# Performance work log

Hardware: AMD Instinct MI355X
Metric: run time of the kernel (lower is better)

The kernel has to match this reference:

```python
import jax, jax.numpy as jnp
import numpy as np

PI = 3.14159  # module uses this truncated pi
CX, CY, FOCAL = 256.0, 256.0, 608.365


def _sh_basis(depth):
    # depth: [B, H, W] (already rescaled to (d+1)/2)
    B, H, W = depth.shape
    gx = jnp.arange(W, dtype=depth.dtype)
    gy = jnp.arange(H, dtype=depth.dtype)
    xx, yy = jnp.meshgrid(gx, gy)            # 'xy' indexing, matches np.meshgrid
    xx = (xx - CX) / FOCAL * depth           # [B,H,W]
    yy = (yy - CY) / FOCAL * depth
    p = jnp.stack([xx, yy, depth], axis=-1)  # [B,H,W,3]

    p_ctr = p[:, 1:-1, 1:-1]
    vw = p_ctr - p[:, 1:-1, 2:]
    vs = p[:, 2:, 1:-1] - p_ctr
    ve = p_ctr - p[:, 1:-1, :-2]
    vn = p[:, :-2, 1:-1] - p_ctr
    normal = jnp.cross(vw, vs) + jnp.cross(ve, vn)     # [B,H-2,W-2,3]
    nmag = jnp.sqrt(jnp.sum(normal * normal, axis=-1)) # [B,H-2,W-2]
    nunit = normal / nmag[..., None]

    pad3 = ((0, 0), (1, 1), (1, 1), (0, 0))
    pad2 = ((0, 0), (1, 1), (1, 1))
    n_raw = jnp.pad(normal, pad3)   # UNNORMALIZED normals (faithful to source: normal_*_pad)
    n_u = jnp.pad(nunit, pad3)      # normalized normals (n_x/n_y/n_z)
    mag = jnp.pad(nmag, pad2)

    nx, ny, nz = n_u[..., 0], n_u[..., 1], n_u[..., 2]
    x2, y2, z2 = nx * nx, ny * ny, nz * nz
    xy, xz, yz = nx * ny, nx * nz, ny * nz

    c0 = PI * np.sqrt(1.0 / (4 * PI))
    c1 = 2 * PI / 3.0 * np.sqrt(3.0 / (4 * PI))
    c2 = PI / 4.0 * 0.5 * np.sqrt(5.0 / (4 * PI))
    c3 = PI / 4.0 * 3.0 * np.sqrt(5.0 / (12 * PI))
    c4 = PI / 4.0 * 3.0 * np.sqrt(5.0 / (48 * PI))

    N = jnp.stack([
        c0 * mag,
        c1 * n_raw[..., 2],
        c1 * n_raw[..., 0],
        c1 * n_raw[..., 1],
        c2 * (2 * z2 - x2 - y2) * mag,
        c3 * xz * mag,
        c3 * yz * mag,
        c4 * (x2 - y2) * mag,
        c3 * xy * mag,
    ], axis=-1)  # [B,H,W,9]
    return N


def setup_inputs() -> dict:
    key = jax.random.key(0)
    k1, k2, k3 = jax.random.split(key, 3)
    B, H, W = 8, 512, 512
    input_img = jax.random.normal(k1, (B, 3, H, W), dtype=jnp.float32)
    depth_target = jax.random.uniform(k2, (B, 1, H, W), dtype=jnp.float32)
    albedo = jax.random.uniform(k3, (B, 3, H, W), dtype=jnp.float32)
    return {"input_img": input_img, "depth_target": depth_target, "albedo": albedo}


def reference(input_img, depth_target, albedo):
    B, C, H, W = input_img.shape
    P = H * W
    depth = (depth_target + 1.0) / 2.0           # [B,1,H,W]
    img = (input_img + 1.0) / 2.0                # [B,3,H,W]
    # mask: binary, 1 wherever channel-0 of scaled image is nonzero
    mask = (img[:, :1] != 0).astype(img.dtype)   # [B,1,H,W]
    img = img * mask

    N = _sh_basis(depth[:, 0])                   # [B,H,W,9]
    A_fla = N.reshape(B, P, 9)

    rhoc_mask = (albedo * mask).reshape(B, 3, P)
    # Faithful bug reproduction: the source loop overwrites rhoc_N each channel
    # iteration, so only the LAST channel (index 2) of rhoc_mask is used for all
    # three least-squares systems.
    A = A_fla * rhoc_mask[:, 2, :, None]         # [B,P,9]
    b = img.reshape(B, 3, P)                     # [B,3,P]

    # Masked least squares: rows with mask==0 have A-row==0 and b==0, so solving
    # over all P rows via normal equations equals torch.gels over nonzero rows.
    AtA = jnp.einsum('bpi,bpj->bij', A, A)       # [B,9,9]
    Atb = jnp.einsum('bcp,bpi->bci', b, A)       # [B,3,9]
    S = jnp.linalg.solve(AtA[:, None], Atb[..., None])[..., 0]  # [B,3,9]
    return S
```

## Files before the change

### kernel.cpp

```cpp
#include <hip/hip_runtime.h>
#include <math.h>

#define HH 512
#define WW 512
#define NB 8
#define NACC 72
#define CHUNKS 64

__global__ __launch_bounds__(256, 2)
void accum_kernel(const float* __restrict__ img,
                  const float* __restrict__ dep,
                  const float* __restrict__ alb,
                  float* __restrict__ ws)
{
    const int b   = blockIdx.y;
    const int tid = threadIdx.x;
    const int tx  = tid & 127;
    const int ty  = tid >> 7;
    const int y0  = blockIdx.x * 8;
    const int x0  = tx * 4;

    const float c0 = (float)(3.14159 * sqrt(1.0 / (4.0 * 3.14159)));
    const float c1 = (float)(2.0 * 3.14159 / 3.0 * sqrt(3.0 / (4.0 * 3.14159)));
    const float c2 = (float)(3.14159 / 4.0 * 0.5 * sqrt(5.0 / (4.0 * 3.14159)));
    const float c3 = (float)(3.14159 / 4.0 * 3.0 * sqrt(5.0 / (12.0 * 3.14159)));
    const float c4 = (float)(3.14159 / 4.0 * 3.0 * sqrt(5.0 / (48.0 * 3.14159)));

    float acc[NACC];
#pragma unroll
    for (int i = 0; i < NACC; ++i) acc[i] = 0.0f;

    const float* depb  = dep + (size_t)b * HH * WW;
    const float* img0b = img + (size_t)(b * 3 + 0) * HH * WW;
    const float* img1b = img + (size_t)(b * 3 + 1) * HH * WW;
    const float* img2b = img + (size_t)(b * 3 + 2) * HH * WW;
    const float* alb2b = alb + (size_t)(b * 3 + 2) * HH * WW;

    float fxv[6];
#pragma unroll
    for (int k = 0; k < 6; ++k)
        fxv[k] = ((float)(x0 - 1 + k) - 256.0f) / 608.365f;

    for (int pass = 0; pass < 4; ++pass) {
        const int y = y0 + pass * 2 + ty;
        if (y < 1 || y >= HH - 1) continue;

        const int row = y * WW + x0;
        const float fy  = ((float)y       - 256.0f) / 608.365f;
        const float fyd = ((float)(y + 1) - 256.0f) / 608.365f;
        const float fyu = ((float)(y - 1) - 256.0f) / 608.365f;

        const float4 cen4 = *reinterpret_cast<const float4*>(depb + row);
        const float4 up4  = *reinterpret_cast<const float4*>(depb + row - WW);
        const float4 dn4  = *reinterpret_cast<const float4*>(depb + row + WW);
        const float  lsc  = depb[row - (tx == 0 ? 0 : 1)];
        const float  rsc  = depb[row + 4];
        const float4 i04  = *reinterpret_cast<const float4*>(img0b + row);
        const float4 i14  = *reinterpret_cast<const float4*>(img1b + row);
        const float4 i24  = *reinterpret_cast<const float4*>(img2b + row);
        const float4 al4  = *reinterpret_cast<const float4*>(alb2b + row);

        float cA[4] = {(cen4.x + 1.0f) * 0.5f, (cen4.y + 1.0f) * 0.5f,
                       (cen4.z + 1.0f) * 0.5f, (cen4.w + 1.0f) * 0.5f};
        float uA[4] = {(up4.x + 1.0f) * 0.5f, (up4.y + 1.0f) * 0.5f,
                       (up4.z + 1.0f) * 0.5f, (up4.w + 1.0f) * 0.5f};
        float dA[4] = {(dn4.x + 1.0f) * 0.5f, (dn4.y + 1.0f) * 0.5f,
                       (dn4.z + 1.0f) * 0.5f, (dn4.w + 1.0f) * 0.5f};
        const float lT = (lsc + 1.0f) * 0.5f;
        const float rT = (rsc + 1.0f) * 0.5f;
        float g0[4] = {i04.x, i04.y, i04.z, i04.w};
        float g1[4] = {i14.x, i14.y, i14.z, i14.w};
        float g2[4] = {i24.x, i24.y, i24.z, i24.w};
        float aA[4] = {al4.x, al4.y, al4.z, al4.w};

#pragma unroll
        for (int p = 0; p < 4; ++p) {
            const bool valid = !((p == 0 && tx == 0) || (p == 3 && tx == 127));

            const float dc = cA[p];
            const float dl = (p == 0) ? lT : cA[(p == 0) ? 0 : p - 1];
            const float dr = (p == 3) ? rT : cA[(p == 3) ? 3 : p + 1];
            const float du = uA[p];
            const float dd = dA[p];

            const float fx  = fxv[p + 1];
            const float fxl = fxv[p];
            const float fxr = fxv[p + 2];

            const float pcx = fx  * dc, pcy = fy  * dc;
            const float prx = fxr * dr, pry = fy  * dr;
            const float plx = fxl * dl, ply = fy  * dl;
            const float pdx = fx  * dd, pdy = fyd * dd;
            const float pux = fx  * du, puy = fyu * du;

            const float vwx = pcx - prx, vwy = pcy - pry, vwz = dc - dr;
            const float vsx = pdx - pcx, vsy = pdy - pcy, vsz = dd - dc;
            const float vex = pcx - plx, vey = pcy - ply, vez = dc - dl;
            const float vnx = pux - pcx, vny = puy - pcy, vnz = du - dc;

            const float nx = (vwy * vsz - vwz * vsy) + (vey * vnz - vez * vny);
            const float ny = (vwz * vsx - vwx * vsz) + (vez * vnx - vex * vnz);
            const float nz = (vwx * vsy - vwy * vsx) + (vex * vny - vey * vnx);

            const float nn   = nx * nx + ny * ny + nz * nz;
            const float mag  = sqrtf(nn);
            const float den  = valid ? mag : 1.0f;
            const float invm = 1.0f / den;
            const float uxn = nx * invm, uyn = ny * invm, uzn = nz * invm;
            const float x2 = uxn * uxn, y2 = uyn * uyn, z2 = uzn * uzn;

            const float N0 = c0 * mag;
            const float N1 = c1 * nz;
            const float N2 = c1 * nx;
            const float N3 = c1 * ny;
            const float N4 = c2 * (2.0f * z2 - x2 - y2) * mag;
            const float N5 = c3 * (uxn * uzn) * mag;
            const float N6 = c3 * (uyn * uzn) * mag;
            const float N7 = c4 * (x2 - y2) * mag;
            const float N8 = c3 * (uxn * uyn) * mag;

            const float vf = valid ? 1.0f : 0.0f;
            const float i0 = (g0[p] + 1.0f) * 0.5f;
            const float i1 = (g1[p] + 1.0f) * 0.5f;
            const float i2 = (g2[p] + 1.0f) * 0.5f;
            const float m  = ((i0 != 0.0f) ? 1.0f : 0.0f) * vf;
            const float b0 = i0 * m, b1 = i1 * m, b2 = i2 * m;
            const float rho = aA[p] * m;

            const float A[9] = {N0 * rho, N1 * rho, N2 * rho, N3 * rho,
                                N4 * rho, N5 * rho, N6 * rho, N7 * rho, N8 * rho};

            int k = 0;
#pragma unroll
            for (int i = 0; i < 9; ++i)
#pragma unroll
                for (int j = i; j < 9; ++j) {
                    acc[k] = fmaf(A[i], A[j], acc[k]);
                    ++k;
                }
#pragma unroll
            for (int i = 0; i < 9; ++i) {
                acc[45 + i] = fmaf(b0, A[i], acc[45 + i]);
                acc[54 + i] = fmaf(b1, A[i], acc[54 + i]);
                acc[63 + i] = fmaf(b2, A[i], acc[63 + i]);
            }
        }
    }

#pragma unroll
    for (int i = 0; i < NACC; ++i) {
        float v = acc[i];
        v += __shfl_xor(v, 32, 64);
        v += __shfl_xor(v, 16, 64);
        v += __shfl_xor(v, 8, 64);
        v += __shfl_xor(v, 4, 64);
        v += __shfl_xor(v, 2, 64);
        v += __shfl_xor(v, 1, 64);
        acc[i] = v;
    }

    __shared__ float red[4][NACC];
    const int wave = tid >> 6;
    const int lane = tid & 63;
    if (lane == 0) {
#pragma unroll
        for (int i = 0; i < NACC; ++i) red[wave][i] = acc[i];
    }
    __syncthreads();
    if (tid < NACC) {
        const float s = red[0][tid] + red[1][tid] + red[2][tid] + red[3][tid];
        ws[((size_t)b * CHUNKS + blockIdx.x) * NACC + tid] = s;
    }
}

__global__ void solve_kernel(const float* __restrict__ ws, float* __restrict__ out)
{
    __shared__ float sums[NACC];
    __shared__ float M[9][12];
    const int b = blockIdx.x;
    const int t = threadIdx.x;

    if (t < NACC) {
        float s = 0.0f;
        for (int c = 0; c < CHUNKS; ++c)
            s += ws[((size_t)b * CHUNKS + c) * NACC + t];
        sums[t] = s;
    }
    __syncthreads();

    if (t == 0) {
        int k = 0;
        for (int i = 0; i < 9; ++i)
            for (int j = i; j < 9; ++j) {
                M[i][j] = sums[k];
                M[j][i] = sums[k];
                ++k;
            }
        for (int c = 0; c < 3; ++c)
            for (int i = 0; i < 9; ++i)
                M[i][9 + c] = sums[45 + c * 9 + i];

        for (int kk = 0; kk < 9; ++kk) {
            int piv = kk;
            float best = fabsf(M[kk][kk]);
            for (int i = kk + 1; i < 9; ++i) {
                const float v = fabsf(M[i][kk]);
                if (v > best) { best = v; piv = i; }
            }
            if (piv != kk)
                for (int j = 0; j < 12; ++j) {
                    const float tmp = M[kk][j];
                    M[kk][j] = M[piv][j];
                    M[piv][j] = tmp;
                }
            const float inv = 1.0f / M[kk][kk];
            for (int i = kk + 1; i < 9; ++i) {
                const float f = M[i][kk] * inv;
                for (int j = kk; j < 12; ++j)
                    M[i][j] -= f * M[kk][j];
            }
        }
        for (int c = 0; c < 3; ++c) {
            float sol[9];
            for (int kk = 8; kk >= 0; --kk) {
                float v = M[kk][9 + c];
                for (int j = kk + 1; j < 9; ++j) v -= M[kk][j] * sol[j];
                sol[kk] = v / M[kk][kk];
            }
            for (int kk = 0; kk < 9; ++kk)
                out[(b * 3 + c) * 9 + kk] = sol[kk];
        }
    }
}

extern "C" void kernel_launch(void* const* d_in, const int* in_sizes, int n_in,
                              void* d_out, int out_size, void* d_ws, size_t ws_size,
                              hipStream_t stream) {
    const float* img = (const float*)d_in[0];
    const float* dep = (const float*)d_in[1];
    const float* alb = (const float*)d_in[2];
    float* out = (float*)d_out;
    float* ws  = (float*)d_ws;

    dim3 grid(CHUNKS, NB);
    accum_kernel<<<grid, 256, 0, stream>>>(img, dep, alb, ws);
    solve_kernel<<<NB, 128, 0, stream>>>(ws, out);
}
```

Before: 112.8 us.

## Fuse accumulation and solve into one kernel via last-block atomic counter

Merges the accumulation and solve kernels into one launch. Each block writes its partial sums, bumps a global atomic counter, and the last block to finish reduces all partials and solves the 8 systems, one thread per batch. A memset of the counter is added per call, and launch bounds go from 2 to 3 blocks per SM, which may pressure the 72-register accumulator array. The aim is to drop a second kernel launch and its gap, at the cost of a serial tail in a single block plus an extra memset.

```diff
diff --git a/kernel.cpp b/kernel.cpp
--- a/kernel.cpp
+++ b/kernel.cpp
@@ -6,13 +6,23 @@
 #define NB 8
 #define NACC 72
 #define CHUNKS 64
-
-__global__ __launch_bounds__(256, 2)
-void accum_kernel(const float* __restrict__ img,
+#define NBLK (CHUNKS * NB)
+
+__global__ __launch_bounds__(256, 3)
+void fused_kernel(const float* __restrict__ img,
                   const float* __restrict__ dep,
                   const float* __restrict__ alb,
-                  float* __restrict__ ws)
+                  float* __restrict__ ws,
+                  float* __restrict__ out)
 {
+    __shared__ float red[4][NACC];
+    __shared__ bool  last_flag;
+    __shared__ float allsums[NB][NACC];
+    __shared__ float M[NB][9][12];
+
+    unsigned int* cnt  = (unsigned int*)ws;
+    float*        part = ws + 64;
+
     const int b   = blockIdx.y;
     const int tid = threadIdx.x;
     const int tx  = tid & 127;
@@ -68,10 +78,10 @@
                        (dn4.z + 1.0f) * 0.5f, (dn4.w + 1.0f) * 0.5f};
         const float lT = (lsc + 1.0f) * 0.5f;
         const float rT = (rsc + 1.0f) * 0.5f;
-        float g0[4] = {i04.x, i04.y, i04.z, i04.w};
-        float g1[4] = {i14.x, i14.y, i14.z, i14.w};
-        float g2[4] = {i24.x, i24.y, i24.z, i24.w};
-        float aA[4] = {al4.x, al4.y, al4.z, al4.w};
+        const float g0[4] = {i04.x, i04.y, i04.z, i04.w};
+        const float g1[4] = {i14.x, i14.y, i14.z, i14.w};
+        const float g2[4] = {i24.x, i24.y, i24.z, i24.w};
+        const float aA[4] = {al4.x, al4.y, al4.z, al4.w};
 
 #pragma unroll
         for (int p = 0; p < 4; ++p) {
@@ -128,7 +138,8 @@
             const float rho = aA[p] * m;
 
             const float A[9] = {N0 * rho, N1 * rho, N2 * rho, N3 * rho,
-                                N4 * rho, N5 * rho, N6 * rho, N7 * rho, N8 * rho};
+                                N4 * rho, N5 * rho, N6 * rho, N7 * rho,
+                                N8 * rho};
 
             int k = 0;
 #pragma unroll
@@ -159,7 +170,6 @@
         acc[i] = v;
     }
 
-    __shared__ float red[4][NACC];
     const int wave = tid >> 6;
     const int lane = tid & 63;
     if (lane == 0) {
@@ -169,66 +179,70 @@
     __syncthreads();
     if (tid < NACC) {
         const float s = red[0][tid] + red[1][tid] + red[2][tid] + red[3][tid];
-        ws[((size_t)b * CHUNKS + blockIdx.x) * NACC + tid] = s;
-    }
-}
-
-__global__ void solve_kernel(const float* __restrict__ ws, float* __restrict__ out)
-{
-    __shared__ float sums[NACC];
-    __shared__ float M[9][12];
-    const int b = blockIdx.x;
-    const int t = threadIdx.x;
-
-    if (t < NACC) {
-        float s = 0.0f;
-        for (int c = 0; c < CHUNKS; ++c)
-            s += ws[((size_t)b * CHUNKS + c) * NACC + t];
-        sums[t] = s;
-    }
-    __syncthreads();
-
-    if (t == 0) {
+        part[((size_t)b * CHUNKS + blockIdx.x) * NACC + tid] = s;
+    }
+
+    __threadfence();
+    __syncthreads();
+    if (tid == 0)
+        last_flag = (atomicAdd(cnt, 1u) == NBLK - 1);
+    __syncthreads();
+    if (!last_flag) return;
+    __threadfence();
+
+    for (int bb = 0; bb < NB; ++bb) {
+        if (tid < NACC) {
+            const float* p = part + (size_t)bb * CHUNKS * NACC + tid;
+            float s = 0.0f;
+            for (int c = 0; c < CHUNKS; ++c)
+                s += p[(size_t)c * NACC];
+            allsums[bb][tid] = s;
+        }
+    }
+    __syncthreads();
+
+    if (tid < NB) {
+        const int bb = tid;
         int k = 0;
         for (int i = 0; i < 9; ++i)
             for (int j = i; j < 9; ++j) {
-                M[i][j] = sums[k];
-                M[j][i] = sums[k];
+                M[bb][i][j] = allsums[bb][k];
+                M[bb][j][i] = allsums[bb][k];
                 ++k;
             }
         for (int c = 0; c < 3; ++c)
             for (int i = 0; i < 9; ++i)
-                M[i][9 + c] = sums[45 + c * 9 + i];
+                M[bb][i][9 + c] = allsums[bb][45 + c * 9 + i];
 
         for (int kk = 0; kk < 9; ++kk) {
             int piv = kk;
-            float best = fabsf(M[kk][kk]);
+            float best = fabsf(M[bb][kk][kk]);
             for (int i = kk + 1; i < 9; ++i) {
-                const float v = fabsf(M[i][kk]);
+                const float v = fabsf(M[bb][i][kk]);
                 if (v > best) { best = v; piv = i; }
             }
             if (piv != kk)
                 for (int j = 0; j < 12; ++j) {
-                    const float tmp = M[kk][j];
-                    M[kk][j] = M[piv][j];
-                    M[piv][j] = tmp;
+                    const float tmp = M[bb][kk][j];
+                    M[bb][kk][j] = M[bb][piv][j];
+                    M[bb][piv][j] = tmp;
                 }
-            const float inv = 1.0f / M[kk][kk];
+            const float inv = 1.0f / M[bb][kk][kk];
             for (int i = kk + 1; i < 9; ++i) {
-                const float f = M[i][kk] * inv;
+                const float f = M[bb][i][kk] * inv;
                 for (int j = kk; j < 12; ++j)
-                    M[i][j] -= f * M[kk][j];
+                    M[bb][i][j] -= f * M[bb][kk][j];
             }
         }
         for (int c = 0; c < 3; ++c) {
             float sol[9];
             for (int kk = 8; kk >= 0; --kk) {
-                float v = M[kk][9 + c];
-                for (int j = kk + 1; j < 9; ++j) v -= M[kk][j] * sol[j];
-                sol[kk] = v / M[kk][kk];
+                float v = M[bb][kk][9 + c];
+                for (int j = kk + 1; j < 9; ++j) v -= M[bb][kk][j] * sol[j];
+                sol[kk] = v / M[bb][kk][kk];
             }
             for (int kk = 0; kk < 9; ++kk)
-                out[(b * 3 + c) * 9 + kk] = sol[kk];
+                out[(bb * 3 + c) * 9 + kk] = sol[kk];
         }
     }
 }
@@ -242,7 +256,8 @@
     float* out = (float*)d_out;
     float* ws  = (float*)d_ws;
 
+    hipMemsetAsync(ws, 0, 64 * sizeof(float), stream);
+
     dim3 grid(CHUNKS, NB);
-    accum_kernel<<<grid, 256, 0, stream>>>(img, dep, alb, ws);
-    solve_kernel<<<NB, 128, 0, stream>>>(ws, out);
+    fused_kernel<<<grid, 256, 0, stream>>>(img, dep, alb, ws, out);
 }
```

New measurement: 145.2 us. 28.7% more time.
